# Kernel tuning notes

Measured on AMD Instinct MI355X. Metric: run time of the kernel, lower is better.

Reference implementation:

```python
import jax, jax.numpy as jnp
import numpy as np

B = 1_048_576
W = 64  # hidden width
N_FREQ = 6   # 3 dims * 6 freqs * (sin,cos) = 36
K_BLOB = 4   # one-blob bins per dim


def _freq_embed(p):
    # [B,3] -> [B,36]
    freqs = 2.0 ** jnp.arange(N_FREQ, dtype=p.dtype)
    ang = jnp.pi * p[:, :, None] * freqs  # [B,3,6]
    return jnp.concatenate([jnp.sin(ang), jnp.cos(ang)], axis=-1).reshape(p.shape[0], 3 * 2 * N_FREQ)


def _sph(d):
    # unit-square parameterization of a direction, [B,3] -> [B,2]
    d = d / (jnp.linalg.norm(d, axis=-1, keepdims=True) + 1e-8)
    u = jnp.arctan2(d[:, 1], d[:, 0]) / (2.0 * jnp.pi) + 0.5
    v = jnp.arccos(jnp.clip(d[:, 2], -1.0 + 1e-6, 1.0 - 1e-6)) / jnp.pi
    return jnp.stack([u, v], axis=-1)


def _one_blob(x, k=K_BLOB):
    # x in [0,1], [B,D] -> [B,D*k] Gaussian one-blob encoding
    centers = (jnp.arange(k, dtype=x.dtype) + 0.5) / k
    sigma = 1.0 / k
    g = jnp.exp(-0.5 * ((x[..., None] - centers) / sigma) ** 2)  # [B,D,k]
    return g.reshape(x.shape[0], -1)


def _encode(p, wi, n, alpha, beta, r):
    ones = jnp.ones((p.shape[0], 2), dtype=p.dtype)
    return jnp.concatenate([
        _freq_embed(p),                      # 36
        _one_blob(_sph(wi)),                 # 8
        _one_blob(_sph(n)),                  # 8
        _one_blob(1.0 - jnp.exp(-r)),        # 4
        alpha, beta,                         # 6
        ones,                                # 2 (implicit bias)
    ], axis=-1)                              # -> [B,64]


def _mlp(x, Ws):
    h = x
    for Wk in Ws[:-1]:
        h = jax.nn.relu(h @ Wk.T)
    return h @ Ws[-1].T  # [B,3]


def setup_inputs() -> dict:
    key = jax.random.key(0)
    ks = jax.random.split(key, 13)
    p = jax.random.normal(ks[0], (B, 3), jnp.float32)
    wi = jax.random.normal(ks[1], (B, 3), jnp.float32)
    n = jax.random.normal(ks[2], (B, 3), jnp.float32)
    alpha = jax.random.uniform(ks[3], (B, 3), jnp.float32)
    beta = jax.random.uniform(ks[4], (B, 3), jnp.float32)
    r = jax.random.uniform(ks[5], (B, 1), jnp.float32)
    s = 1.0 / np.sqrt(W)
    weights = {}
    for i in range(6):
        weights[f"W{i}"] = jax.random.normal(ks[6 + i], (W, W), jnp.float32) * s
    weights["W6"] = jax.random.normal(ks[12], (3, W), jnp.float32) * s
    return dict(p=p, wi=wi, n=n, alpha=alpha, beta=beta, r=r, **weights)


def reference(p, wi, n, alpha, beta, r, W0, W1, W2, W3, W4, W5, W6):
    x = _encode(p, wi, n, alpha, beta, r)
    out = _mlp(x, [W0, W1, W2, W3, W4, W5, W6])
    return out * (alpha + beta)  # reflectance factorization
```

## Files before the change

### kernel.cpp

```cpp
#include <hip/hip_runtime.h>


typedef _Float16 f16;
typedef f16 f16x2 __attribute__((ext_vector_type(2)));
typedef f16 f16x4 __attribute__((ext_vector_type(4)));
typedef f16 f16x8 __attribute__((ext_vector_type(8)));
typedef float f32x4 __attribute__((ext_vector_type(4)));

#define MFMA32(A, B, C) __builtin_amdgcn_mfma_f32_16x16x32_f16(A, B, C, 0, 0, 0)

static constexpr int TILES  = 4;
static constexpr int WAVES  = 8;
static constexpr int BLOCK  = WAVES * 64;
static constexpr int ROUNDS = 8;
static constexpr int SPB    = ROUNDS * 4 * 64;

static constexpr int    WUNITS   = 50;
static constexpr int    WCHUNKS  = WUNITS * 64;
static constexpr size_t WS_BYTES = (size_t)WCHUNKS * 16;
static constexpr int    LDS_WEI  = WUNITS * 1024;
static constexpr int    LDS_STG  = 4 * 4096;
static constexpr int    LDS_TOT  = LDS_WEI + LDS_STG;

__host__ __device__ __forceinline__ int tau(int x) {
    return (x & 32) + ((x & 7) >> 2) * 16 + ((x >> 3) & 3) * 4 + (x & 3);
}

__device__ __forceinline__ f16x2 pkh(float a, float b) {
    return __builtin_bit_cast(f16x2, __builtin_amdgcn_cvt_pkrtz(a, b));
}

__device__ __forceinline__ f16x4 cat22(f16x2 a, f16x2 b) {
    return __builtin_shufflevector(a, b, 0, 1, 2, 3);
}

__device__ __forceinline__ f16x8 cat44(f16x4 a, f16x4 b) {
    return __builtin_shufflevector(a, b, 0, 1, 2, 3, 4, 5, 6, 7);
}

__device__ __forceinline__ f16x4 pack4(f32x4 v) {
    return cat22(pkh(v[0], v[1]), pkh(v[2], v[3]));
}

__device__ __forceinline__ float fast_atan2_rev(float y, float x) {
    const float ax = __builtin_fabsf(x), ay = __builtin_fabsf(y);
    const float mx = fmaxf(ax, ay), mn = fminf(ax, ay);
    const float a = mn * __builtin_amdgcn_rcpf(fmaxf(mx, 1e-30f));
    const float s = a * a;
    float r = a * (0.99997726f + s * (-0.33262347f + s * (0.19354346f +
              s * (-0.11643287f + s * (0.05265332f - s * 0.01172120f)))));
    if (ay > ax) r = 1.5707963268f - r;
    if (x < 0.0f) r = 3.1415926536f - r;
    r = (y < 0.0f) ? -r : r;
    return r * 0.15915494309189535f;
}

__device__ __forceinline__ float fast_acos(float x) {
    const float ax = __builtin_fabsf(x);
    const float t = __builtin_amdgcn_sqrtf(1.0f - ax);
    const float p = t * (1.5707288f + ax * (-0.2121144f +
                    ax * (0.0742610f - ax * 0.0187293f)));
    return (x < 0.0f) ? (3.1415926536f - p) : p;
}

__device__ __forceinline__ void blob4(float x, float* out) {
    const float dx = x - 0.125f;
    const float E0 = __expf(-8.0f * dx * dx);
    const float R  = __expf(4.0f * dx);
    const float t1 = R * 0.60653066f;
    const float t2 = R * 0.22313016f;
    const float t3 = R * 0.082084999f;
    out[0] = E0;
    out[1] = E0 * t1;
    out[2] = out[1] * t2;
    out[3] = out[2] * t3;
}

__device__ __forceinline__ f16x8 make_wchunk(
    int c, const float* __restrict__ W0, const float* __restrict__ W1,
    const float* __restrict__ W2, const float* __restrict__ W3,
    const float* __restrict__ W4, const float* __restrict__ W5,
    const float* __restrict__ W6)
{
    const int lane2 = c & 63;
    const int unit  = c >> 6;
    const int q = lane2 >> 4, m = lane2 & 15;
    f16x8 v;
    if (unit < 48) {
        const int l = unit >> 3, kt = (unit & 7) >> 2, mt = unit & 3;
        const float* Ws[6] = {W0, W1, W2, W3, W4, W5};
        const float* __restrict__ Wl = Ws[l];
#pragma unroll
        for (int j = 0; j < 8; ++j) {
            const int x = kt * 32 + q * 8 + j;
            const int src = (l == 0) ? x : tau(x);
            v[j] = (f16)Wl[(mt * 16 + m) * 64 + src];
        }
    } else {
        const int kt = unit - 48;
#pragma unroll
        for (int j = 0; j < 8; ++j) {
            const int src = tau(kt * 32 + q * 8 + j);
            v[j] = (m < 3) ? (f16)W6[m * 64 + src] : (f16)0.0f;
        }
    }
    return v;
}

__global__ __launch_bounds__(256, 1) void pack_weights_kernel(
    const float* __restrict__ W0, const float* __restrict__ W1,
    const float* __restrict__ W2, const float* __restrict__ W3,
    const float* __restrict__ W4, const float* __restrict__ W5,
    const float* __restrict__ W6, f16* __restrict__ ws)
{
    const int c = (int)blockIdx.x * 256 + threadIdx.x;
    if (c >= WCHUNKS) return;
    *(f16x8*)(ws + (size_t)c * 8) = make_wchunk(c, W0, W1, W2, W3, W4, W5, W6);
}

__device__ __forceinline__ void async_ld16(const void* g, void* l) {
    __builtin_amdgcn_global_load_lds(
        (const __attribute__((address_space(1))) void*)g,
        (__attribute__((address_space(3))) void*)l,
        16, 0, 0);
}

template<int PACKED>
__global__ __launch_bounds__(BLOCK, 4) void nrc_mlp_kernel(
    const float* __restrict__ P,  const float* __restrict__ WI,
    const float* __restrict__ NV, const float* __restrict__ AL,
    const float* __restrict__ BE, const float* __restrict__ RR,
    const f16*   __restrict__ ws,
    const float* __restrict__ W0, const float* __restrict__ W1,
    const float* __restrict__ W2, const float* __restrict__ W3,
    const float* __restrict__ W4, const float* __restrict__ W5,
    const float* __restrict__ W6, float* __restrict__ Out)
{
    __shared__ __attribute__((aligned(16))) unsigned char smem[LDS_TOT];

    const int tid  = threadIdx.x;
    const int lane = tid & 63;
    const int w    = tid >> 6;
    const int q    = lane >> 4;
    const int m    = lane & 15;
    const bool producer = (w < 4);
    const int  cw  = w & 3;
    const int  blk_base = (int)blockIdx.x * SPB;

    unsigned char* const stg = smem + LDS_WEI;

    if (PACKED) {
#pragma unroll
        for (int i = 0; i < (WCHUNKS + BLOCK - 1) / BLOCK; ++i) {
            const int c = i * BLOCK + tid;
            if (c < WCHUNKS)
                async_ld16(ws + (size_t)c * 8, smem + c * 16);
        }
    } else {
#pragma unroll
        for (int i = 0; i < (WCHUNKS + BLOCK - 1) / BLOCK; ++i) {
            const int c = i * BLOCK + tid;
            if (c < WCHUNKS)
                *(f16x8*)(smem + c * 16) = make_wchunk(c, W0, W1, W2, W3, W4, W5, W6);
        }
    }

    const f16x4 zero4 = {(f16)0.0f, (f16)0.0f, (f16)0.0f, (f16)0.0f};
    const f32x4 ZF = {0.0f, 0.0f, 0.0f, 0.0f};
    unsigned char* const wb = smem + lane * 16;

    f16x8 bf[TILES][2];

    auto compute = [&](int rr) {
        __builtin_amdgcn_s_setprio(1);
#pragma unroll
        for (int layer = 0; layer < 6; ++layer) {
            f16x8 wa[8];
#pragma unroll
            for (int f = 0; f < 8; ++f)
                wa[f] = *(const f16x8*)(wb + (layer * 8 + f) * 1024);

#pragma unroll
            for (int t = 0; t < TILES; ++t) {
                f32x4 acc[4];
#pragma unroll
                for (int mt = 0; mt < 4; ++mt) {
                    f32x4 z = MFMA32(wa[mt], bf[t][0], ZF);
                    z = MFMA32(wa[4 + mt], bf[t][1], z);
                    acc[mt] = z;
                }
                f16x4 pk[4];
#pragma unroll
                for (int mt = 0; mt < 4; ++mt)
                    pk[mt] = __builtin_elementwise_max(pack4(acc[mt]), zero4);
                bf[t][0] = cat44(pk[0], pk[1]);
                bf[t][1] = cat44(pk[2], pk[3]);
            }
        }
        __builtin_amdgcn_s_setprio(0);
        const f16x8 w6f0 = *(const f16x8*)(wb + 48 * 1024);
        const f16x8 w6f1 = *(const f16x8*)(wb + 49 * 1024);
        const int rbase = blk_base + rr * 256 + cw * 64;
        float aa[TILES][3];
#pragma unroll
        for (int t = 0; t < TILES; ++t) {
            const int s = rbase + t * 16 + m;
#pragma unroll
            for (int d = 0; d < 3; ++d)
                aa[t][d] = AL[s * 3 + d] + BE[s * 3 + d];
        }
#pragma unroll
        for (int t = 0; t < TILES; ++t) {
            f32x4 z = MFMA32(w6f0, bf[t][0], ZF);
            z = MFMA32(w6f1, bf[t][1], z);
            if (lane < 16) {
                const int s = rbase + t * 16 + m;
                float* o = Out + s * 3;
                o[0] = z[0] * aa[t][0];
                o[1] = z[1] * aa[t][1];
                o[2] = z[2] * aa[t][2];
            }
        }
    };

    for (int r = 0; r < ROUNDS; ++r) {
        f16x2 hf[32];
        if (producer) {
            const int s = blk_base + r * 256 + cw * 64 + lane;

            float pv[3], wv[3], nv[3], av[3], bv[3];
#pragma unroll
            for (int d = 0; d < 3; ++d) {
                pv[d] = P [s * 3 + d];
                wv[d] = WI[s * 3 + d];
                nv[d] = NV[s * 3 + d];
                av[d] = AL[s * 3 + d];
                bv[d] = BE[s * 3 + d];
            }
            const float rv = RR[s];

#pragma unroll
            for (int d = 0; d < 3; ++d) {
                float sA[6], cA[6];
                const float fr = __builtin_amdgcn_fractf(pv[d] * 0.5f);
                sA[0] = __builtin_amdgcn_sinf(fr);
                cA[0] = __builtin_amdgcn_cosf(fr);
#pragma unroll
                for (int k = 1; k < 6; ++k) {
                    const float s2 = sA[k-1] * sA[k-1];
                    const float sc = sA[k-1] * cA[k-1];
                    cA[k] = fmaf(-2.0f, s2, 1.0f);
                    sA[k] = sc + sc;
                }
                hf[d * 6 + 0] = pkh(sA[0], sA[1]);
                hf[d * 6 + 1] = pkh(sA[2], sA[3]);
                hf[d * 6 + 2] = pkh(sA[4], sA[5]);
                hf[d * 6 + 3] = pkh(cA[0], cA[1]);
                hf[d * 6 + 4] = pkh(cA[2], cA[3]);
                hf[d * 6 + 5] = pkh(cA[4], cA[5]);
            }
#pragma unroll
            for (int which = 0; which < 2; ++which) {
                const float* dv = (which == 0) ? wv : nv;
                const int ho = 18 + which * 4;
                const float nr = __builtin_amdgcn_sqrtf(dv[0]*dv[0] + dv[1]*dv[1] + dv[2]*dv[2]) + 1e-8f;
                const float u  = fast_atan2_rev(dv[1], dv[0]) + 0.5f;
                float zc = dv[2] * __builtin_amdgcn_rcpf(nr);
                zc = fminf(fmaxf(zc, -1.0f + 1e-6f), 1.0f - 1e-6f);
                const float vv = fast_acos(zc) * 0.3183098861837907f;
                float ob[8];
                blob4(u,  &ob[0]);
                blob4(vv, &ob[4]);
                hf[ho + 0] = pkh(ob[0], ob[1]);
                hf[ho + 1] = pkh(ob[2], ob[3]);
                hf[ho + 2] = pkh(ob[4], ob[5]);
                hf[ho + 3] = pkh(ob[6], ob[7]);
            }
            {
                float ob[4];
                blob4(1.0f - __expf(-rv), ob);
                hf[26] = pkh(ob[0], ob[1]);
                hf[27] = pkh(ob[2], ob[3]);
            }
            hf[28] = pkh(av[0], av[1]);
            hf[29] = pkh(av[2], bv[0]);
            hf[30] = pkh(bv[1], bv[2]);
            hf[31] = pkh(1.0f, 1.0f);
        } else if (r > 0) {
            compute(r - 1);
        }

#pragma unroll
        for (int h = 0; h < 2; ++h) {
            __syncthreads();
            if (producer && ((lane >> 5) == h)) {
                unsigned char* const tb =
                    stg + cw * 4096 + ((lane >> 4) & 1) * 2048 + m * 128;
#pragma unroll
                for (int g = 0; g < 8; ++g) {
                    const int slot0 = (4 * g + 4 * m) & 31;
                    *(f16x8*)(tb + slot0 * 4) =
                        cat44(cat22(hf[g*4 + 0], hf[g*4 + 1]),
                              cat22(hf[g*4 + 2], hf[g*4 + 3]));
                }
            }
            __syncthreads();
            if (!producer) {
#pragma unroll
                for (int t2 = 0; t2 < 2; ++t2) {
#pragma unroll
                    for (int kt = 0; kt < 2; ++kt) {
                        const int s0 = (16 * kt + 4 * q + 4 * m) & 31;
                        bf[h * 2 + t2][kt] = *(const f16x8*)(
                            stg + cw * 4096 + t2 * 2048 + m * 128 + s0 * 4);
                    }
                }
            }
        }
    }
    if (!producer) compute(ROUNDS - 1);
}

extern "C" void kernel_launch(void* const* d_in, const int* in_sizes, int n_in,
                              void* d_out, int out_size, void* d_ws, size_t ws_size,
                              hipStream_t stream) {
    (void)n_in; (void)out_size;
    const float* P  = (const float*)d_in[0];
    const float* WI = (const float*)d_in[1];
    const float* NV = (const float*)d_in[2];
    const float* AL = (const float*)d_in[3];
    const float* BE = (const float*)d_in[4];
    const float* RR = (const float*)d_in[5];
    const float* W0 = (const float*)d_in[6];
    const float* W1 = (const float*)d_in[7];
    const float* W2 = (const float*)d_in[8];
    const float* W3 = (const float*)d_in[9];
    const float* W4 = (const float*)d_in[10];
    const float* W5 = (const float*)d_in[11];
    const float* W6 = (const float*)d_in[12];
    f16*   ws  = (f16*)d_ws;
    float* Out = (float*)d_out;

    const int Bn = in_sizes[0] / 3;
    const int grid = Bn / SPB;

    if (ws_size >= WS_BYTES) {
        hipLaunchKernelGGL(pack_weights_kernel, dim3((WCHUNKS + 255) / 256),
                           dim3(256), 0, stream, W0, W1, W2, W3, W4, W5, W6, ws);
        hipLaunchKernelGGL((nrc_mlp_kernel<1>), dim3(grid), dim3(BLOCK), 0, stream,
                           P, WI, NV, AL, BE, RR, ws,
                           W0, W1, W2, W3, W4, W5, W6, Out);
    } else {
        hipLaunchKernelGGL((nrc_mlp_kernel<0>), dim3(grid), dim3(BLOCK), 0, stream,
                           P, WI, NV, AL, BE, RR, ws,
                           W0, W1, W2, W3, W4, W5, W6, Out);
    }
}
```

Baseline: 179.6 us.

## Stream layer-0 weights from global, shrink LDS, and simplify producer staging

```diff
diff --git a/kernel.cpp b/kernel.cpp
--- a/kernel.cpp
+++ b/kernel.cpp
@@ -12,14 +12,17 @@
 static constexpr int TILES  = 4;
 static constexpr int WAVES  = 8;
 static constexpr int BLOCK  = WAVES * 64;
+static constexpr int PAIRS  = 4;
 static constexpr int ROUNDS = 8;
-static constexpr int SPB    = ROUNDS * 4 * 64;
+static constexpr int SPB    = ROUNDS * PAIRS * 64;
 
 static constexpr int    WUNITS   = 50;
 static constexpr int    WCHUNKS  = WUNITS * 64;
 static constexpr size_t WS_BYTES = (size_t)WCHUNKS * 16;
-static constexpr int    LDS_WEI  = WUNITS * 1024;
-static constexpr int    LDS_STG  = 4 * 4096;
+static constexpr int    LDSUNITS = 42;
+static constexpr int    LDSCHNK  = LDSUNITS * 64;
+static constexpr int    LDS_WEI  = LDSUNITS * 1024;
+static constexpr int    LDS_STG  = PAIRS * 8192;
 static constexpr int    LDS_TOT  = LDS_WEI + LDS_STG;
 
 __host__ __device__ __forceinline__ int tau(int x) {
@@ -143,64 +146,93 @@
     const int w    = tid >> 6;
     const int q    = lane >> 4;
     const int m    = lane & 15;
-    const bool producer = (w < 4);
-    const int  cw  = w & 3;
+    const bool prod = (w < PAIRS);
+    const int  p    = prod ? w : (w - PAIRS);
     const int  blk_base = (int)blockIdx.x * SPB;
 
-    unsigned char* const stg = smem + LDS_WEI;
+    unsigned char* const stgp = smem + LDS_WEI + p * 8192;
+    unsigned char* const wbl  = smem + lane * 16;
 
     if (PACKED) {
 #pragma unroll
-        for (int i = 0; i < (WCHUNKS + BLOCK - 1) / BLOCK; ++i) {
+        for (int i = 0; i < 6; ++i) {
             const int c = i * BLOCK + tid;
-            if (c < WCHUNKS)
-                async_ld16(ws + (size_t)c * 8, smem + c * 16);
+            if (c < LDSCHNK)
+                async_ld16(ws + (size_t)(512 + c) * 8, smem + c * 16);
         }
     } else {
 #pragma unroll
-        for (int i = 0; i < (WCHUNKS + BLOCK - 1) / BLOCK; ++i) {
+        for (int i = 0; i < 6; ++i) {
             const int c = i * BLOCK + tid;
-            if (c < WCHUNKS)
-                *(f16x8*)(smem + c * 16) = make_wchunk(c, W0, W1, W2, W3, W4, W5, W6);
+            if (c < LDSCHNK)
+                *(f16x8*)(smem + c * 16) =
+                    make_wchunk(512 + c, W0, W1, W2, W3, W4, W5, W6);
         }
     }
 
     const f16x4 zero4 = {(f16)0.0f, (f16)0.0f, (f16)0.0f, (f16)0.0f};
     const f32x4 ZF = {0.0f, 0.0f, 0.0f, 0.0f};
-    unsigned char* const wb = smem + lane * 16;
 
     f16x8 bf[TILES][2];
 
     auto compute = [&](int rr) {
         __builtin_amdgcn_s_setprio(1);
+        f32x4 acc[TILES][4];
 #pragma unroll
         for (int layer = 0; layer < 6; ++layer) {
-            f16x8 wa[8];
-#pragma unroll
-            for (int f = 0; f < 8; ++f)
-                wa[f] = *(const f16x8*)(wb + (layer * 8 + f) * 1024);
-
+            f16x8 wa[4];
+            if (layer == 0) {
+                if (PACKED) {
+#pragma unroll
+                    for (int mt = 0; mt < 4; ++mt)
+                        wa[mt] = *(const f16x8*)(ws + (size_t)(mt * 64 + lane) * 8);
+                } else {
+#pragma unroll
+                    for (int mt = 0; mt < 4; ++mt)
+                        wa[mt] = make_wchunk(mt * 64 + lane, W0, W1, W2, W3, W4, W5, W6);
+                }
+            } else {
+#pragma unroll
+                for (int mt = 0; mt < 4; ++mt)
+                    wa[mt] = *(const f16x8*)(wbl + ((layer - 1) * 8 + mt) * 1024);
+            }
+#pragma unroll
+            for (int t = 0; t < TILES; ++t)
+#pragma unroll
+                for (int mt = 0; mt < 4; ++mt)
+                    acc[t][mt] = MFMA32(wa[mt], bf[t][0], ZF);
+            if (layer == 0) {
+                if (PACKED) {
+#pragma unroll
+                    for (int mt = 0; mt < 4; ++mt)
+                        wa[mt] = *(const f16x8*)(ws + (size_t)((4 + mt) * 64 + lane) * 8);
+                } else {
+#pragma unroll
+                    for (int mt = 0; mt < 4; ++mt)
+                        wa[mt] = make_wchunk((4 + mt) * 64 + lane, W0, W1, W2, W3, W4, W5, W6);
+                }
+            } else {
+#pragma unroll
+                for (int mt = 0; mt < 4; ++mt)
+                    wa[mt] = *(const f16x8*)(wbl + ((layer - 1) * 8 + 4 + mt) * 1024);
+            }
+#pragma unroll
+            for (int t = 0; t < TILES; ++t)
+#pragma unroll
+                for (int mt = 0; mt < 4; ++mt)
+                    acc[t][mt] = MFMA32(wa[mt], bf[t][1], acc[t][mt]);
 #pragma unroll
             for (int t = 0; t < TILES; ++t) {
-                f32x4 acc[4];
-#pragma unroll
-                for (int mt = 0; mt < 4; ++mt) {
-                    f32x4 z = MFMA32(wa[mt], bf[t][0], ZF);
-                    z = MFMA32(wa[4 + mt], bf[t][1], z);
-                    acc[mt] = z;
-                }
                 f16x4 pk[4];
 #pragma unroll
                 for (int mt = 0; mt < 4; ++mt)
-                    pk[mt] = __builtin_elementwise_max(pack4(acc[mt]), zero4);
+                    pk[mt] = __builtin_elementwise_max(pack4(acc[t][mt]), zero4);
                 bf[t][0] = cat44(pk[0], pk[1]);
                 bf[t][1] = cat44(pk[2], pk[3]);
             }
         }
         __builtin_amdgcn_s_setprio(0);
-        const f16x8 w6f0 = *(const f16x8*)(wb + 48 * 1024);
-        const f16x8 w6f1 = *(const f16x8*)(wb + 49 * 1024);
-        const int rbase = blk_base + rr * 256 + cw * 64;
+        const int rbase = blk_base + rr * (PAIRS * 64) + p * 64;
         float aa[TILES][3];
 #pragma unroll
         for (int t = 0; t < TILES; ++t) {
@@ -209,40 +241,53 @@
             for (int d = 0; d < 3; ++d)
                 aa[t][d] = AL[s * 3 + d] + BE[s * 3 + d];
         }
+        f32x4 oz[TILES];
+        {
+            const f16x8 w6a = *(const f16x8*)(wbl + 40 * 1024);
+#pragma unroll
+            for (int t = 0; t < TILES; ++t) oz[t] = MFMA32(w6a, bf[t][0], ZF);
+            const f16x8 w6b = *(const f16x8*)(wbl + 41 * 1024);
+#pragma unroll
+            for (int t = 0; t < TILES; ++t) oz[t] = MFMA32(w6b, bf[t][1], oz[t]);
+        }
 #pragma unroll
         for (int t = 0; t < TILES; ++t) {
-            f32x4 z = MFMA32(w6f0, bf[t][0], ZF);
-            z = MFMA32(w6f1, bf[t][1], z);
             if (lane < 16) {
                 const int s = rbase + t * 16 + m;
                 float* o = Out + s * 3;
-                o[0] = z[0] * aa[t][0];
-                o[1] = z[1] * aa[t][1];
-                o[2] = z[2] * aa[t][2];
+                o[0] = oz[t][0] * aa[t][0];
+                o[1] = oz[t][1] * aa[t][1];
+                o[2] = oz[t][2] * aa[t][2];
             }
         }
     };
 
     for (int r = 0; r < ROUNDS; ++r) {
-        f16x2 hf[32];
-        if (producer) {
-            const int s = blk_base + r * 256 + cw * 64 + lane;
-
-            float pv[3], wv[3], nv[3], av[3], bv[3];
-#pragma unroll
-            for (int d = 0; d < 3; ++d) {
-                pv[d] = P [s * 3 + d];
-                wv[d] = WI[s * 3 + d];
-                nv[d] = NV[s * 3 + d];
-                av[d] = AL[s * 3 + d];
-                bv[d] = BE[s * 3 + d];
-            }
-            const float rv = RR[s];
+        if (prod) {
+#pragma unroll
+            for (int t = 0; t < TILES; ++t) {
+                bf[t][0] = f16x8{};
+                bf[t][1] = f16x8{};
+            }
+            const int s = blk_base + r * (PAIRS * 64) + p * 64 + lane;
+            unsigned char* const myrow = stgp + lane * 128;
+            const int rot = (lane * 4) & 31;
+            auto put = [&](int D, f16x2 a, f16x2 b) {
+                *(f16x4*)(myrow + (((D + rot) & 31) << 2)) = cat22(a, b);
+            };
+
+            const float3 pv = *(const float3*)(P  + 3 * s);
+            const float3 wv = *(const float3*)(WI + 3 * s);
+            const float3 nv = *(const float3*)(NV + 3 * s);
+            const float3 av = *(const float3*)(AL + 3 * s);
+            const float3 bv = *(const float3*)(BE + 3 * s);
+            const float  rv = RR[s];
+            const float parr[3] = {pv.x, pv.y, pv.z};
 
 #pragma unroll
             for (int d = 0; d < 3; ++d) {
                 float sA[6], cA[6];
-                const float fr = __builtin_amdgcn_fractf(pv[d] * 0.5f);
+                const float fr = __builtin_amdgcn_fractf(parr[d] * 0.5f);
                 sA[0] = __builtin_amdgcn_sinf(fr);
                 cA[0] = __builtin_amdgcn_cosf(fr);
 #pragma unroll
@@ -252,73 +297,54 @@
                     cA[k] = fmaf(-2.0f, s2, 1.0f);
                     sA[k] = sc + sc;
                 }
-                hf[d * 6 + 0] = pkh(sA[0], sA[1]);
-                hf[d * 6 + 1] = pkh(sA[2], sA[3]);
-                hf[d * 6 + 2] = pkh(sA[4], sA[5]);
-                hf[d * 6 + 3] = pkh(cA[0], cA[1]);
-                hf[d * 6 + 4] = pkh(cA[2], cA[3]);
-                hf[d * 6 + 5] = pkh(cA[4], cA[5]);
+                put(6 * d + 0, pkh(sA[0], sA[1]), pkh(sA[2], sA[3]));
+                put(6 * d + 2, pkh(sA[4], sA[5]), pkh(cA[0], cA[1]));
+                put(6 * d + 4, pkh(cA[2], cA[3]), pkh(cA[4], cA[5]));
             }
 #pragma unroll
             for (int which = 0; which < 2; ++which) {
-                const float* dv = (which == 0) ? wv : nv;
-                const int ho = 18 + which * 4;
-                const float nr = __builtin_amdgcn_sqrtf(dv[0]*dv[0] + dv[1]*dv[1] + dv[2]*dv[2]) + 1e-8f;
-                const float u  = fast_atan2_rev(dv[1], dv[0]) + 0.5f;
-                float zc = dv[2] * __builtin_amdgcn_rcpf(nr);
+                const float3 dv3 = (which == 0) ? wv : nv;
+                const float dx = dv3.x, dy = dv3.y, dz = dv3.z;
+                const int D0 = 18 + which * 4;
+                const float nr = __builtin_amdgcn_sqrtf(dx*dx + dy*dy + dz*dz) + 1e-8f;
+                const float u  = fast_atan2_rev(dy, dx) + 0.5f;
+                float zc = dz * __builtin_amdgcn_rcpf(nr);
                 zc = fminf(fmaxf(zc, -1.0f + 1e-6f), 1.0f - 1e-6f);
                 const float vv = fast_acos(zc) * 0.3183098861837907f;
                 float ob[8];
                 blob4(u,  &ob[0]);
                 blob4(vv, &ob[4]);
-                hf[ho + 0] = pkh(ob[0], ob[1]);
-                hf[ho + 1] = pkh(ob[2], ob[3]);
-                hf[ho + 2] = pkh(ob[4], ob[5]);
-                hf[ho + 3] = pkh(ob[6], ob[7]);
+                put(D0,     pkh(ob[0], ob[1]), pkh(ob[2], ob[3]));
+                put(D0 + 2, pkh(ob[4], ob[5]), pkh(ob[6], ob[7]));
             }
             {
                 float ob[4];
                 blob4(1.0f - __expf(-rv), ob);
-                hf[26] = pkh(ob[0], ob[1]);
-                hf[27] = pkh(ob[2], ob[3]);
-            }
-            hf[28] = pkh(av[0], av[1]);
-            hf[29] = pkh(av[2], bv[0]);
-            hf[30] = pkh(bv[1], bv[2]);
-            hf[31] = pkh(1.0f, 1.0f);
+                put(26, pkh(ob[0], ob[1]), pkh(ob[2], ob[3]));
+            }
+            put(28, pkh(av.x, av.y), pkh(av.z, bv.x));
+            put(30, pkh(bv.y, bv.z), pkh(1.0f, 1.0f));
         } else if (r > 0) {
             compute(r - 1);
         }
 
-#pragma unroll
-        for (int h = 0; h < 2; ++h) {
-            __syncthreads();
-            if (producer && ((lane >> 5) == h)) {
-                unsigned char* const tb =
-                    stg + cw * 4096 + ((lane >> 4) & 1) * 2048 + m * 128;
-#pragma unroll
-                for (int g = 0; g < 8; ++g) {
-                    const int slot0 = (4 * g + 4 * m) & 31;
-                    *(f16x8*)(tb + slot0 * 4) =
-                        cat44(cat22(hf[g*4 + 0], hf[g*4 + 1]),
-                              cat22(hf[g*4 + 2], hf[g*4 + 3]));
+        __syncthreads();
+
+        if (!prod) {
+#pragma unroll
+            for (int t = 0; t < TILES; ++t) {
+                const int n = t * 16 + m;
+#pragma unroll
+                for (int kt = 0; kt < 2; ++kt) {
+                    const int s0 = (16 * kt + 4 * q + 4 * m) & 31;
+                    bf[t][kt] = *(const f16x8*)(stgp + n * 128 + (s0 << 2));
                 }
             }
-            __syncthreads();
-            if (!producer) {
-#pragma unroll
-                for (int t2 = 0; t2 < 2; ++t2) {
-#pragma unroll
-                    for (int kt = 0; kt < 2; ++kt) {
-                        const int s0 = (16 * kt + 4 * q + 4 * m) & 31;
-                        bf[h * 2 + t2][kt] = *(const f16x8*)(
-                            stg + cw * 4096 + t2 * 2048 + m * 128 + s0 * 4);
-                    }
-                }
-            }
-        }
+        }
+
+        __syncthreads();
     }
-    if (!producer) compute(ROUNDS - 1);
+    if (!prod) compute(ROUNDS - 1);
 }
 
 extern "C" void kernel_launch(void* const* d_in, const int* in_sizes, int n_in,
```

Result: faster. 173.8 us (-3.2%).
